# Kernel tuning notes

Hardware: AMD Instinct MI355X
Metric: run time of the kernel (lower is better)

The kernel has to match this reference:

```python
import jax, jax.numpy as jnp
import numpy as np

EPS = 1e-3  # keras LayerNormalization default epsilon

def layer_norm(x, gamma, beta):
    mu = jnp.mean(x, axis=-1, keepdims=True)
    var = jnp.var(x, axis=-1, keepdims=True)
    return (x - mu) * jax.lax.rsqrt(var + EPS) * gamma + beta

def setup_inputs() -> dict:
    key = jax.random.key(0)
    ks = jax.random.split(key, 10)
    B, N, FD, AD, PD, DP = 4, 512, 256, 256, 128, 64
    s = lambda k, *sh: jax.random.normal(k, sh, dtype=jnp.float32)
    return {
        "F": s(ks[0], B, N, FD),
        "D": s(ks[1], B, N, N, DP),
        "Wq": s(ks[2], FD, AD) / np.sqrt(FD),
        "Wk": s(ks[3], FD, AD) / np.sqrt(FD),
        "Wv": s(ks[4], FD, AD) / np.sqrt(FD),
        "g_f": jnp.ones((FD,), jnp.float32),
        "b_f": jnp.zeros((FD,), jnp.float32),
        "g_p": jnp.ones((DP,), jnp.float32),
        "b_p": jnp.zeros((DP,), jnp.float32),
        "W_pt": s(ks[5], DP, PD) / np.sqrt(DP),
        "b_pt": jnp.zeros((PD,), jnp.float32),
        "W_ph": s(ks[6], PD, 1) / np.sqrt(PD),
    }

def reference(F, D, Wq, Wk, Wv, g_f, b_f, g_p, b_p, W_pt, b_pt, W_ph):
    # features path
    Fn = layer_norm(F, g_f, b_f)                       # [B,N,FD]
    Q = Fn @ Wq                                        # [B,N,AD]
    K = Fn @ Wk
    V = Fn @ Wv
    # pair-bias path: LN -> Dense(pairs_dim)+bias -> Dense(num_heads=1)
    Bn = layer_norm(D, g_p, b_p)                       # [B,N,N,DP]
    Bt = Bn @ W_pt + b_pt                              # [B,N,N,PD]
    bias = (Bt @ W_ph)[..., 0]                         # [B,N,N]
    scalar = 1.0 / jnp.sqrt(jnp.float32(Q.shape[-1]))
    A = jnp.einsum('bqd,bkd->bqk', Q, K) + bias        # QK^T + pair bias
    A = jax.nn.softmax(scalar * A, axis=-1)
    O = jnp.einsum('bqk,bkd->bqd', A, V)               # [B,N,AD]
    return jnp.sum(O, axis=-1)                         # [B,N]
```

## Files before the change

### kernel.cpp

```cpp
#include <hip/hip_runtime.h>
#include <cstddef>
#include <cstdint>

#define OFF_GW    0
#define OFF_WV    64
#define OFF_SC    320
#define OFF_VSUM  384
#define OFF_Q     2432
#define OFF_K     526720

typedef float v4f __attribute__((ext_vector_type(4)));

__device__ __forceinline__ void load_lds_16B(const float* g, float* l) {
  __builtin_amdgcn_global_load_lds(
      (const __attribute__((address_space(1))) uint32_t*)g,
      (__attribute__((address_space(3))) uint32_t*)l, 16, 0, 0);
}

__global__ __launch_bounds__(256) void k0_consts(
    const float* __restrict__ Wv, const float* __restrict__ g_p,
    const float* __restrict__ b_p, const float* __restrict__ W_pt,
    const float* __restrict__ b_pt, const float* __restrict__ W_ph,
    float* __restrict__ ws) {
  int t = threadIdx.x;
  if (blockIdx.x < 64) {
    int row = blockIdx.x * 4 + (t >> 6);
    int l = t & 63;
    float s = 0.f;
#pragma unroll
    for (int j = 0; j < 4; ++j) s += Wv[row * 256 + l + 64 * j];
    for (int m = 32; m >= 1; m >>= 1) s += __shfl_xor(s, m);
    if (l == 0) ws[OFF_WV + row] = s;
  } else {
    __shared__ float wc_s[64];
    __shared__ float wph_s[128];
    if (t < 128) wph_s[t] = W_ph[t];
    __syncthreads();
    int c = t >> 2, sub = t & 3;
    float wc = 0.f;
#pragma unroll
    for (int j = 0; j < 32; ++j)
      wc += W_pt[c * 128 + sub * 32 + j] * wph_s[sub * 32 + j];
    wc += __shfl_xor(wc, 1);
    wc += __shfl_xor(wc, 2);
    if (sub == 0) {
      wc_s[c] = wc;
      ws[OFF_GW + c] = g_p[c] * wc;
    }
    __syncthreads();
    if (t == 0) {
      float sg = 0.f, bc = 0.f;
      for (int cc = 0; cc < 64; ++cc) {
        sg += g_p[cc] * wc_s[cc];
        bc += b_p[cc] * wc_s[cc];
      }
      for (int p = 0; p < 128; ++p) bc += b_pt[p] * wph_s[p];
      ws[OFF_SC] = sg;
      ws[OFF_SC + 1] = bc;
    }
  }
}

__global__ __launch_bounds__(256) void k1_ln_qk(
    const float* __restrict__ F, const float* __restrict__ Wq,
    const float* __restrict__ Wk, const float* __restrict__ g_f,
    const float* __restrict__ b_f, float* __restrict__ ws) {
  __shared__ __align__(16) float fn[8][260];
  __shared__ float smu[8], srn[8];
  int t = threadIdx.x;
  int g = blockIdx.x >> 1, h = blockIdx.x & 1;
  int row0 = g * 8;
  const float* Fp = F + (size_t)row0 * 256;
#pragma unroll
  for (int k = 0; k < 8; ++k) fn[k][t] = Fp[k * 256 + t];
  __syncthreads();
  int r = t >> 5, l32 = t & 31;
  float s1 = 0.f, s2 = 0.f;
#pragma unroll
  for (int m = 0; m < 8; ++m) {
    float x = fn[r][l32 + 32 * m];
    s1 += x;
    s2 += x * x;
  }
  for (int m = 16; m >= 1; m >>= 1) {
    s1 += __shfl_xor(s1, m);
    s2 += __shfl_xor(s2, m);
  }
  if (l32 == 0) {
    float mu = s1 * (1.f / 256.f);
    float var = s2 * (1.f / 256.f) - mu * mu;
    smu[r] = mu;
    srn[r] = rsqrtf(var + 1e-3f);
  }
  __syncthreads();
  float gf = g_f[t], bf = b_f[t];
#pragma unroll
  for (int k = 0; k < 8; ++k)
    fn[k][t] = (fn[k][t] - smu[k]) * srn[k] * gf + bf;
  __syncthreads();
  if (h == 0) {
    const float* wv = ws + OFF_WV;
    float s = 0.f;
#pragma unroll
    for (int m = 0; m < 8; ++m) s += fn[r][l32 + 32 * m] * wv[l32 + 32 * m];
    for (int m = 16; m >= 1; m >>= 1) s += __shfl_xor(s, m);
    if (l32 == 0) ws[OFF_VSUM + row0 + r] = s;
  }
  int matsel = t >> 7;
  int col = h * 128 + (t & 127);
  const float* W = matsel ? Wk : Wq;
  float acc[8] = {0, 0, 0, 0, 0, 0, 0, 0};
#pragma unroll 2
  for (int f = 0; f < 256; f += 4) {
    float w0 = W[(f + 0) * 256 + col];
    float w1 = W[(f + 1) * 256 + col];
    float w2 = W[(f + 2) * 256 + col];
    float w3 = W[(f + 3) * 256 + col];
#pragma unroll
    for (int k = 0; k < 8; ++k) {
      v4f x = *(const v4f*)(&fn[k][f]);
      acc[k] = fmaf(x.w, w3,
               fmaf(x.z, w2, fmaf(x.y, w1, fmaf(x.x, w0, acc[k]))));
    }
  }
  float* Out = ws + (matsel ? OFF_K : OFF_Q) + (size_t)row0 * 256 + col;
#pragma unroll
  for (int k = 0; k < 8; ++k) Out[k * 256] = acc[k];
}

__global__ __launch_bounds__(256) void kb_bias_attn(
    const float* __restrict__ D, const float* __restrict__ ws,
    float* __restrict__ out) {
  __shared__ __align__(16) float stage[4][2][1024];
  __shared__ float Sx[4][512];
  __shared__ __align__(16) float Qs[4][256];
  __shared__ float vs[512];
  int t = threadIdx.x;
  int w = t >> 6, l = t & 63;
  int b = blockIdx.x >> 7, tile = blockIdx.x & 127;
  int rowbase = b * 512 + tile * 4;

#pragma unroll
  for (int k = 0; k < 4; ++k)
    Qs[k][t] = ws[OFF_Q + (size_t)(rowbase + k) * 256 + t];
  vs[t] = ws[OFF_VSUM + b * 512 + t];
  vs[t + 256] = ws[OFF_VSUM + b * 512 + 256 + t];
  float sum_gw = ws[OFF_SC];
  float bconst = ws[OFF_SC + 1];
  int qq = l & 3, e4 = l >> 2;
  v4f g_rot[4];
#pragma unroll
  for (int j = 0; j < 4; ++j) {
    int p = (e4 + j) & 3;
    g_rot[j] = *(const v4f*)(ws + OFF_GW + qq * 16 + p * 4);
  }
  __syncthreads();

  const float* Dw = D + (size_t)(rowbase + w) * 512 * 64;
  float* buf0 = &stage[w][0][0];
  float* buf1 = &stage[w][1][0];
#pragma unroll
  for (int j = 0; j < 4; ++j)
    load_lds_16B(Dw + j * 256 + l * 4, buf0 + j * 256);

  for (int i = 0; i < 32; ++i) {
    float* cur = (i & 1) ? buf1 : buf0;
    float* nxt = (i & 1) ? buf0 : buf1;
    if (i + 1 < 32) {
#pragma unroll
      for (int j = 0; j < 4; ++j)
        load_lds_16B(Dw + (i + 1) * 1024 + j * 256 + l * 4, nxt + j * 256);
      __builtin_amdgcn_s_waitcnt(0x0F74);
    } else {
      __builtin_amdgcn_s_waitcnt(0x0F70);
    }
    asm volatile("" ::: "memory");
    const float* ebase = cur + e4 * 64 + qq * 16;
    float s1 = 0.f, s2 = 0.f, sw = 0.f;
#pragma unroll
    for (int j = 0; j < 4; ++j) {
      int p = (e4 + j) & 3;
      v4f x = *(const v4f*)(ebase + p * 4);
      s1 += x.x + x.y + x.z + x.w;
      s2 += x.x * x.x + x.y * x.y + x.z * x.z + x.w * x.w;
      sw += x.x * g_rot[j].x + x.y * g_rot[j].y + x.z * g_rot[j].z +
            x.w * g_rot[j].w;
    }
    s1 += __shfl_xor(s1, 1);
    s2 += __shfl_xor(s2, 1);
    sw += __shfl_xor(sw, 1);
    s1 += __shfl_xor(s1, 2);
    s2 += __shfl_xor(s2, 2);
    sw += __shfl_xor(sw, 2);
    if (qq == 0) {
      float mu = s1 * (1.f / 64.f);
      float var = s2 * (1.f / 64.f) - mu * mu;
      float rn = rsqrtf(var + 1e-3f);
      Sx[w][i * 16 + e4] = (rn * (sw - mu * sum_gw) + bconst) * 0.0625f;
    }
  }
  __syncthreads();

  const float* Kg = ws + OFF_K;
  const v4f* K0p = (const v4f*)(Kg + (size_t)(b * 512 + t) * 256);
  const v4f* K1p = (const v4f*)(Kg + (size_t)(b * 512 + 256 + t) * 256);
  float a0[4] = {0, 0, 0, 0}, a1[4] = {0, 0, 0, 0};
#pragma unroll 8
  for (int f = 0; f < 64; ++f) {
    v4f kv0 = K0p[f];
    v4f kv1 = K1p[f];
#pragma unroll
    for (int rr = 0; rr < 4; ++rr) {
      v4f qv = *(const v4f*)(&Qs[rr][f * 4]);
      a0[rr] += qv.x * kv0.x + qv.y * kv0.y + qv.z * kv0.z + qv.w * kv0.w;
      a1[rr] += qv.x * kv1.x + qv.y * kv1.y + qv.z * kv1.z + qv.w * kv1.w;
    }
  }
#pragma unroll
  for (int rr = 0; rr < 4; ++rr) {
    Sx[rr][t] += a0[rr] * 0.0625f;
    Sx[rr][t + 256] += a1[rr] * 0.0625f;
  }
  __syncthreads();

  float m = -1e30f;
#pragma unroll
  for (int j = 0; j < 8; ++j) m = fmaxf(m, Sx[w][l + 64 * j]);
  for (int mm = 32; mm >= 1; mm >>= 1) m = fmaxf(m, __shfl_xor(m, mm));
  float se = 0.f, sv = 0.f;
#pragma unroll
  for (int j = 0; j < 8; ++j) {
    float ev = __expf(Sx[w][l + 64 * j] - m);
    se += ev;
    sv += ev * vs[l + 64 * j];
  }
  for (int mm = 32; mm >= 1; mm >>= 1) {
    se += __shfl_xor(se, mm);
    sv += __shfl_xor(sv, mm);
  }
  if (l == 0) out[rowbase + w] = sv / se;
}

extern "C" void kernel_launch(void* const* d_in, const int* in_sizes, int n_in,
                              void* d_out, int out_size, void* d_ws,
                              size_t ws_size, hipStream_t stream) {
  const float* F    = (const float*)d_in[0];
  const float* D    = (const float*)d_in[1];
  const float* Wq   = (const float*)d_in[2];
  const float* Wk   = (const float*)d_in[3];
  const float* Wv   = (const float*)d_in[4];
  const float* g_f  = (const float*)d_in[5];
  const float* b_f  = (const float*)d_in[6];
  const float* g_p  = (const float*)d_in[7];
  const float* b_p  = (const float*)d_in[8];
  const float* W_pt = (const float*)d_in[9];
  const float* b_pt = (const float*)d_in[10];
  const float* W_ph = (const float*)d_in[11];
  float* out = (float*)d_out;
  float* ws = (float*)d_ws;

  k0_consts<<<65, 256, 0, stream>>>(Wv, g_p, b_p, W_pt, b_pt, W_ph, ws);
  k1_ln_qk<<<512, 256, 0, stream>>>(F, Wq, Wk, g_f, b_f, ws);
  kb_bias_attn<<<512, 256, 0, stream>>>(D, ws, out);
}
```

Baseline: 439.2 us.

## Read pair tensor directly into registers, one pair row per lane

Replaces the double-buffered global-to-LDS staging of the pair tensor D with direct per-thread vector loads. Each lane now holds a full 64-channel pair row (16 float4) in registers, so the layer-norm and bias reductions need no cross-lane shuffles. This removes the LDS traffic, the waitcnt pipeline and the shuffles. In exchange, each lane reads a 256-byte strided row, which makes the global loads less coalesced per instruction, and register pressure rises from holding 16 x and 16 g vectors.

Result: no change. 443.1 us (+0.9%).

```diff
diff --git a/kernel.cpp b/kernel.cpp
--- a/kernel.cpp
+++ b/kernel.cpp
@@ -10,12 +10,6 @@
 #define OFF_K     526720
 
 typedef float v4f __attribute__((ext_vector_type(4)));
-
-__device__ __forceinline__ void load_lds_16B(const float* g, float* l) {
-  __builtin_amdgcn_global_load_lds(
-      (const __attribute__((address_space(1))) uint32_t*)g,
-      (__attribute__((address_space(3))) uint32_t*)l, 16, 0, 0);
-}
 
 __global__ __launch_bounds__(256) void k0_consts(
     const float* __restrict__ Wv, const float* __restrict__ g_p,
@@ -131,7 +125,6 @@
 __global__ __launch_bounds__(256) void kb_bias_attn(
     const float* __restrict__ D, const float* __restrict__ ws,
     float* __restrict__ out) {
-  __shared__ __align__(16) float stage[4][2][1024];
   __shared__ float Sx[4][512];
   __shared__ __align__(16) float Qs[4][256];
   __shared__ float vs[512];
@@ -147,57 +140,29 @@
   vs[t + 256] = ws[OFF_VSUM + b * 512 + 256 + t];
   float sum_gw = ws[OFF_SC];
   float bconst = ws[OFF_SC + 1];
-  int qq = l & 3, e4 = l >> 2;
-  v4f g_rot[4];
-#pragma unroll
-  for (int j = 0; j < 4; ++j) {
-    int p = (e4 + j) & 3;
-    g_rot[j] = *(const v4f*)(ws + OFF_GW + qq * 16 + p * 4);
-  }
-  __syncthreads();
-
-  const float* Dw = D + (size_t)(rowbase + w) * 512 * 64;
-  float* buf0 = &stage[w][0][0];
-  float* buf1 = &stage[w][1][0];
-#pragma unroll
-  for (int j = 0; j < 4; ++j)
-    load_lds_16B(Dw + j * 256 + l * 4, buf0 + j * 256);
-
-  for (int i = 0; i < 32; ++i) {
-    float* cur = (i & 1) ? buf1 : buf0;
-    float* nxt = (i & 1) ? buf0 : buf1;
-    if (i + 1 < 32) {
-#pragma unroll
-      for (int j = 0; j < 4; ++j)
-        load_lds_16B(Dw + (i + 1) * 1024 + j * 256 + l * 4, nxt + j * 256);
-      __builtin_amdgcn_s_waitcnt(0x0F74);
-    } else {
-      __builtin_amdgcn_s_waitcnt(0x0F70);
-    }
-    asm volatile("" ::: "memory");
-    const float* ebase = cur + e4 * 64 + qq * 16;
+  v4f g[16];
+#pragma unroll
+  for (int p = 0; p < 16; ++p) g[p] = *(const v4f*)(ws + OFF_GW + p * 4);
+
+  const float* Dw = D + (size_t)(rowbase + w) * (512 * 64);
+#pragma unroll 1
+  for (int i = 0; i < 8; ++i) {
+    const v4f* e = (const v4f*)(Dw + (size_t)(i * 64 + l) * 64);
+    v4f x[16];
+#pragma unroll
+    for (int p = 0; p < 16; ++p) x[p] = e[p];
     float s1 = 0.f, s2 = 0.f, sw = 0.f;
 #pragma unroll
-    for (int j = 0; j < 4; ++j) {
-      int p = (e4 + j) & 3;
-      v4f x = *(const v4f*)(ebase + p * 4);
-      s1 += x.x + x.y + x.z + x.w;
-      s2 += x.x * x.x + x.y * x.y + x.z * x.z + x.w * x.w;
-      sw += x.x * g_rot[j].x + x.y * g_rot[j].y + x.z * g_rot[j].z +
-            x.w * g_rot[j].w;
-    }
-    s1 += __shfl_xor(s1, 1);
-    s2 += __shfl_xor(s2, 1);
-    sw += __shfl_xor(sw, 1);
-    s1 += __shfl_xor(s1, 2);
-    s2 += __shfl_xor(s2, 2);
-    sw += __shfl_xor(sw, 2);
-    if (qq == 0) {
-      float mu = s1 * (1.f / 64.f);
-      float var = s2 * (1.f / 64.f) - mu * mu;
-      float rn = rsqrtf(var + 1e-3f);
-      Sx[w][i * 16 + e4] = (rn * (sw - mu * sum_gw) + bconst) * 0.0625f;
-    }
+    for (int p = 0; p < 16; ++p) {
+      v4f xx = x[p];
+      s1 += xx.x + xx.y + xx.z + xx.w;
+      s2 += xx.x * xx.x + xx.y * xx.y + xx.z * xx.z + xx.w * xx.w;
+      sw += xx.x * g[p].x + xx.y * g[p].y + xx.z * g[p].z + xx.w * g[p].w;
+    }
+    float mu = s1 * (1.f / 64.f);
+    float var = s2 * (1.f / 64.f) - mu * mu;
+    float rn = rsqrtf(var + 1e-3f);
+    Sx[w][i * 64 + l] = (rn * (sw - mu * sum_gw) + bconst) * 0.0625f;
   }
   __syncthreads();
 
```
